# Kernel optimization log

Hardware: AMD Instinct MI355X
Metric: run time of the kernel (lower is better)

## Reference

```python
import jax, jax.numpy as jnp
import numpy as np

NUM_HEADS = 8
NUM_GROUPS = 8
EPS = 1e-5


def group_norm(x, scale, bias):
    # x: [B, C, H, W]; GroupNorm with NUM_GROUPS groups, per-channel affine.
    B, C, H, W = x.shape
    xg = x.reshape(B, NUM_GROUPS, C // NUM_GROUPS, H, W)
    mean = jnp.mean(xg, axis=(2, 3, 4), keepdims=True)
    var = jnp.var(xg, axis=(2, 3, 4), keepdims=True)
    xg = (xg - mean) * jax.lax.rsqrt(var + EPS)
    xn = xg.reshape(B, C, H, W)
    return xn * scale[None, :, None, None] + bias[None, :, None, None]


def setup_inputs() -> dict:
    key = jax.random.key(0)
    ks = jax.random.split(key, 4)
    B, C, H, W = 8, 256, 32, 32
    x = jax.random.normal(ks[0], (B, C, H, W), dtype=jnp.float32)
    gn_scale = jnp.ones((C,), dtype=jnp.float32)
    gn_bias = jnp.zeros((C,), dtype=jnp.float32)
    w_qkv = jax.random.normal(ks[1], (3 * C, C), dtype=jnp.float32) * (1.0 / np.sqrt(C))
    b_qkv = jnp.zeros((3 * C,), dtype=jnp.float32)
    w_out = jax.random.normal(ks[2], (C, C), dtype=jnp.float32) * (1.0 / np.sqrt(C))
    b_out = jnp.zeros((C,), dtype=jnp.float32)
    return {"x": x, "gn_scale": gn_scale, "gn_bias": gn_bias,
            "w_qkv": w_qkv, "b_qkv": b_qkv, "w_out": w_out, "b_out": b_out}


def reference(x, gn_scale, gn_bias, w_qkv, b_qkv, w_out, b_out):
    B, C, H, W = x.shape
    hd = C // NUM_HEADS  # head_dim
    N = H * W

    h = group_norm(x, gn_scale, gn_bias)
    # 1x1 conv == channel matmul: [B, 3C, H, W]
    qkv = jnp.einsum('oc,bchw->bohw', w_qkv, h) + b_qkv[None, :, None, None]
    q, k, v = jnp.split(qkv, 3, axis=1)
    # [B, heads, head_dim, N]
    q = q.reshape(B, NUM_HEADS, hd, N)
    k = k.reshape(B, NUM_HEADS, hd, N)
    v = v.reshape(B, NUM_HEADS, hd, N)

    scale = 1.0 / np.sqrt(hd).astype(np.float32)
    attn = jnp.einsum('bhdn,bhdm->bhnm', q, k) * scale  # [B, h, N, N]
    attn = jax.nn.softmax(attn, axis=-1)
    out = jnp.einsum('bhnm,bhdm->bhdn', attn, v)  # [B, h, hd, N]
    out = out.reshape(B, C, H, W)
    out = jnp.einsum('oc,bchw->bohw', w_out, out) + b_out[None, :, None, None]
    return x + out
```

## Files before the change

### kernel.cpp

```cpp
#include <hip/hip_runtime.h>
#include <hip/hip_bf16.h>
#include <math.h>

#define BB 8
#define CC 256
#define NN 1024
#define HEADS 8
#define HDIM 32
#define NGRP 8

using bf16x8 = __attribute__((ext_vector_type(8))) short;
using f32x4  = __attribute__((ext_vector_type(4))) float;

#if __has_builtin(__builtin_amdgcn_exp2f)
#define EXP2(x) __builtin_amdgcn_exp2f(x)
#else
#define EXP2(x) exp2f(x)
#endif

#define SCL_Q_LOG2E 0.2550348892803828f

static __device__ __forceinline__ ushort f2bf(float x) {
  union { __hip_bfloat16 b; ushort u; } c;
  c.b = __float2bfloat16(x);
  return c.u;
}

__global__ __launch_bounds__(256) void gn_stats1(
    const float* __restrict__ x, float2* __restrict__ part)
{
  const int p = blockIdx.x, t = threadIdx.x;
  const float4* src = (const float4*)x + (size_t)p * 512;
  const float4 a = src[t], b = src[t + 256];
  float s  = a.x + a.y + a.z + a.w + b.x + b.y + b.z + b.w;
  float ss = a.x*a.x + a.y*a.y + a.z*a.z + a.w*a.w
           + b.x*b.x + b.y*b.y + b.z*b.z + b.w*b.w;
#pragma unroll
  for (int off = 32; off > 0; off >>= 1) {
    s  += __shfl_down(s, off);
    ss += __shfl_down(ss, off);
  }
  __shared__ float rs[4], rss[4];
  const int wid = t >> 6, lane = t & 63;
  if (lane == 0) { rs[wid] = s; rss[wid] = ss; }
  __syncthreads();
  if (t == 0) {
    float2 o;
    o.x = rs[0] + rs[1] + rs[2] + rs[3];
    o.y = rss[0] + rss[1] + rss[2] + rss[3];
    part[p] = o;
  }
}

__global__ __launch_bounds__(256) void gnt_kernel(
    const float* __restrict__ x, const float2* __restrict__ part,
    const float* __restrict__ gns, const float* __restrict__ gnb,
    ushort* __restrict__ hT)
{
  __shared__ ushort Ls[64 * 68];
  __shared__ float2 gstat[2];
  const int t = threadIdx.x;
  const int b = blockIdx.z;
  const int c0 = blockIdx.y << 6, n0 = blockIdx.x << 6;

  if (t < 32) {
    const int gsel = t >> 4, ci = t & 15;
    const float2 pp = part[((b * 8) + (blockIdx.y << 1) + gsel) * 16 + ci];
    float s = pp.x, ss = pp.y;
#pragma unroll
    for (int off = 8; off > 0; off >>= 1) {
      s  += __shfl_down(s, off, 16);
      ss += __shfl_down(ss, off, 16);
    }
    if (ci == 0) {
      const float mean = s * (1.f / 32768.f);
      const float var = ss * (1.f / 32768.f) - mean * mean;
      float2 o; o.x = mean; o.y = rsqrtf(var + 1e-5f);
      gstat[gsel] = o;
    }
  }
  __syncthreads();

#pragma unroll
  for (int li = 0; li < 4; ++li) {
    const int id = t + (li << 8);
    const int row = id >> 4, col4 = id & 15;
    const int c = c0 + row;
    const float2 st = gstat[row >> 5];
    const float sc = gns[c] * st.y;
    const float sh = gnb[c] - st.x * sc;
    const float4 v = *(const float4*)(x + ((size_t)b * CC + c) * NN + n0 + col4 * 4);
    const int nb = col4 * 4;
    Ls[(nb + 0) * 68 + row] = f2bf(v.x * sc + sh);
    Ls[(nb + 1) * 68 + row] = f2bf(v.y * sc + sh);
    Ls[(nb + 2) * 68 + row] = f2bf(v.z * sc + sh);
    Ls[(nb + 3) * 68 + row] = f2bf(v.w * sc + sh);
  }
  __syncthreads();
#pragma unroll
  for (int li = 0; li < 2; ++li) {
    const int id = t + (li << 8);
    const int nR = id >> 3, cP = id & 7;
    union { uint4 v; ushort4 s[2]; } ov;
    ov.s[0] = *(const ushort4*)&Ls[nR * 68 + cP * 8];
    ov.s[1] = *(const ushort4*)&Ls[nR * 68 + cP * 8 + 4];
    *(uint4*)(hT + ((size_t)b * NN + n0 + nR) * CC + c0 + cP * 8) = ov.v;
  }
}

template <int MODE>
__global__ __launch_bounds__(256) void conv_mfma_kernel(
    const float* __restrict__ W32, const float* __restrict__ bias,
    const ushort* __restrict__ X, const float* __restrict__ xres,
    ushort* __restrict__ qT2, ushort* __restrict__ kT2, ushort* __restrict__ vN,
    float* __restrict__ out)
{
  const int t = threadIdx.x;
  const int w = t >> 6, l = t & 63;
  const int lg = l >> 4, lr = l & 15;
  const int wr = w >> 1, wc = w & 1;
  const int b = blockIdx.z;
  const int o0 = blockIdx.y << 6, n0 = blockIdx.x << 6;

  __shared__ ushort Ws[64][72];
  __shared__ ushort Xs[64][72];

  union FragU { ushort4 u[2]; bf16x8 f; };
  f32x4 acc[2][2] = {};

  const ushort* Xb = X + (size_t)b * 1024 * 256;

  for (int k0 = 0; k0 < 256; k0 += 64) {
    __syncthreads();
#pragma unroll
    for (int li = 0; li < 2; ++li) {
      const int id = t + (li << 8);
      const int rr = id >> 3, c8 = id & 7;
      const float* wsrc = W32 + (size_t)(o0 + rr) * 256 + k0 + c8 * 8;
      const float4 wa = *(const float4*)wsrc;
      const float4 wb = *(const float4*)(wsrc + 4);
      union { uint4 v; ushort s[8]; } wv;
      wv.s[0] = f2bf(wa.x); wv.s[1] = f2bf(wa.y); wv.s[2] = f2bf(wa.z); wv.s[3] = f2bf(wa.w);
      wv.s[4] = f2bf(wb.x); wv.s[5] = f2bf(wb.y); wv.s[6] = f2bf(wb.z); wv.s[7] = f2bf(wb.w);
      *(uint4*)&Ws[rr][c8 * 8] = wv.v;
      const uint4 xv = *(const uint4*)(Xb + (size_t)(n0 + rr) * 256 + k0 + c8 * 8);
      *(uint4*)&Xs[rr][c8 * 8] = xv;
    }
    __syncthreads();

    FragU af[2][2], xf[2][2];
#pragma unroll
    for (int i = 0; i < 2; ++i)
#pragma unroll
      for (int kc = 0; kc < 2; ++kc) {
        const ushort* p = &Ws[wr * 32 + i * 16 + lr][kc * 32 + lg * 4];
        af[i][kc].u[0] = *(const ushort4*)p;
        af[i][kc].u[1] = *(const ushort4*)(p + 16);
        const ushort* q = &Xs[wc * 32 + i * 16 + lr][kc * 32 + lg * 4];
        xf[i][kc].u[0] = *(const ushort4*)q;
        xf[i][kc].u[1] = *(const ushort4*)(q + 16);
      }
#pragma unroll
    for (int ms = 0; ms < 2; ++ms)
#pragma unroll
      for (int ns = 0; ns < 2; ++ns) {
        acc[ms][ns] = __builtin_amdgcn_mfma_f32_16x16x32_bf16(af[ms][0].f, xf[ns][0].f, acc[ms][ns], 0, 0, 0);
        acc[ms][ns] = __builtin_amdgcn_mfma_f32_16x16x32_bf16(af[ms][1].f, xf[ns][1].f, acc[ms][ns], 0, 0, 0);
      }
  }

  if (MODE == 0) {
    const int sec = o0 >> 8;
    const int oin = o0 & 255;
    const float scl = (sec == 0) ? SCL_Q_LOG2E : 1.0f;
    ushort* Lp = &Xs[0][0];
    __syncthreads();
#pragma unroll
    for (int ms = 0; ms < 2; ++ms) {
      const int ob = o0 + wr * 32 + ms * 16 + lg * 4;
      const float4 b4 = *(const float4*)(bias + ob);
      const int ol = wr * 32 + ms * 16 + lg * 4;
#pragma unroll
      for (int ns = 0; ns < 2; ++ns) {
        const int nl = wc * 32 + ns * 16 + lr;
        Lp[(ol + 0) * 68 + nl] = f2bf((acc[ms][ns][0] + b4.x) * scl);
        Lp[(ol + 1) * 68 + nl] = f2bf((acc[ms][ns][1] + b4.y) * scl);
        Lp[(ol + 2) * 68 + nl] = f2bf((acc[ms][ns][2] + b4.z) * scl);
        Lp[(ol + 3) * 68 + nl] = f2bf((acc[ms][ns][3] + b4.w) * scl);
      }
    }
    __syncthreads();
    if (sec < 2) {
      ushort* dst = (sec == 0) ? qT2 : kT2;
      const int nl = t & 63, hd = t >> 6;
      const int hl = hd >> 1, dh = hd & 1;
      const int bh = b * 8 + (oin >> 5) + hl;
      union { uint4 v[2]; ushort s[16]; } o;
#pragma unroll
      for (int j = 0; j < 16; ++j)
        o.s[j] = Lp[(hl * 32 + dh * 16 + j) * 68 + nl];
      uint4* dp = (uint4*)(dst + (((size_t)bh * 2 + dh) * 1024 + n0 + nl) * 16);
      dp[0] = o.v[0];
      dp[1] = o.v[1];
    } else {
      const int r = t >> 2, p = t & 3;
      const int oo = oin + r, hh = oo >> 5, d0 = oo & 31;
      union { uint4 v[2]; ushort4 s[4]; } o;
#pragma unroll
      for (int j = 0; j < 4; ++j)
        o.s[j] = *(const ushort4*)&Lp[r * 68 + p * 16 + j * 4];
      uint4* dp = (uint4*)(vN + (((size_t)b * 8 + hh) * 32 + d0) * 1024 + n0 + p * 16);
      dp[0] = o.v[0];
      dp[1] = o.v[1];
    }
  } else {
#pragma unroll
    for (int ms = 0; ms < 2; ++ms) {
      const int ob = o0 + wr * 32 + ms * 16 + lg * 4;
      const float4 b4 = *(const float4*)(bias + ob);
#pragma unroll
      for (int ns = 0; ns < 2; ++ns) {
        const int n = n0 + wc * 32 + ns * 16 + lr;
        const size_t i0 = ((size_t)b * 256 + ob) * 1024 + n;
        out[i0]          = acc[ms][ns][0] + b4.x + xres[i0];
        out[i0 + 1024]   = acc[ms][ns][1] + b4.y + xres[i0 + 1024];
        out[i0 + 2048]   = acc[ms][ns][2] + b4.z + xres[i0 + 2048];
        out[i0 + 3072]   = acc[ms][ns][3] + b4.w + xres[i0 + 3072];
      }
    }
  }
}

__global__ __launch_bounds__(128) void attn_kernel(
    const ushort* __restrict__ qT2, const ushort* __restrict__ kT2,
    const ushort* __restrict__ vN, ushort* __restrict__ aoT)
{
  const int t = threadIdx.x;
  const int w = t >> 6, l = t & 63;
  const int lg = l >> 4, lr = l & 15;
  const int bh = blockIdx.y;
  const int b = bh >> 3, hh = bh & 7;
  const int qbase = blockIdx.x << 6;

  __shared__ ushort Ks[64][40];
  __shared__ ushort Vs[32][72];

  union FragU { ushort4 u[2]; bf16x8 f; };

  const ushort* Qb2 = qT2 + (size_t)bh * 2 * 1024 * 16;
  const ushort* Kb2 = kT2 + (size_t)bh * 2 * 1024 * 16;
  const ushort* Vbh = vN + (size_t)bh * 32 * 1024;

  FragU qf[2];
#pragma unroll
  for (int qh = 0; qh < 2; ++qh) {
    const int qn = qbase + w * 32 + qh * 16 + lr;
    qf[qh].u[0] = *(const ushort4*)(Qb2 + (size_t)qn * 16 + lg * 4);
    qf[qh].u[1] = *(const ushort4*)(Qb2 + (size_t)(1024 + qn) * 16 + lg * 4);
  }

  f32x4 accO[2][2] = {};
  float lsum0 = 0.f, lsum1 = 0.f;

  const int km = t >> 1, kh = t & 1;
  const ushort* kbase = Kb2 + ((size_t)kh * 1024 + km) * 16;
  const int vd = t >> 2, vp = (t & 3) * 16;
  const ushort* vbase = Vbh + (size_t)vd * 1024 + vp;

  uint4 kr0 = *(const uint4*)kbase;
  uint4 kr1 = *(const uint4*)(kbase + 8);
  uint4 vr0 = *(const uint4*)vbase;
  uint4 vr1 = *(const uint4*)(vbase + 8);

  for (int m0 = 0; m0 < NN; m0 += 64) {
    __syncthreads();
    *(uint4*)&Ks[km][kh * 16] = kr0;
    *(uint4*)&Ks[km][kh * 16 + 8] = kr1;
    *(uint4*)&Vs[vd][vp] = vr0;
    *(uint4*)&Vs[vd][vp + 8] = vr1;
    __syncthreads();

    if (m0 + 64 < NN) {
      const ushort* kn = kbase + (size_t)(m0 + 64) * 16;
      kr0 = *(const uint4*)kn;
      kr1 = *(const uint4*)(kn + 8);
      const ushort* vn2 = vbase + (m0 + 64);
      vr0 = *(const uint4*)vn2;
      vr1 = *(const uint4*)(vn2 + 8);
    }

    f32x4 s[4][2];
#pragma unroll
    for (int ms = 0; ms < 4; ++ms) {
      FragU kf;
      const ushort* kp = &Ks[ms * 16 + lr][lg * 4];
      kf.u[0] = *(const ushort4*)kp;
      kf.u[1] = *(const ushort4*)(kp + 16);
      f32x4 z = {0.f, 0.f, 0.f, 0.f};
      s[ms][0] = __builtin_amdgcn_mfma_f32_16x16x32_bf16(kf.f, qf[0].f, z, 0, 0, 0);
      s[ms][1] = __builtin_amdgcn_mfma_f32_16x16x32_bf16(kf.f, qf[1].f, z, 0, 0, 0);
    }

    bf16x8 pb[2][2];
#pragma unroll
    for (int mc = 0; mc < 2; ++mc) {
      bf16x8 f0, f1;
#pragma unroll
      for (int r = 0; r < 4; ++r) {
        const float a0 = EXP2(s[2 * mc][0][r]);
        const float a1 = EXP2(s[2 * mc + 1][0][r]);
        const float b0 = EXP2(s[2 * mc][1][r]);
        const float b1 = EXP2(s[2 * mc + 1][1][r]);
        lsum0 += a0 + a1;
        lsum1 += b0 + b1;
        f0[r] = (short)f2bf(a0); f0[r + 4] = (short)f2bf(a1);
        f1[r] = (short)f2bf(b0); f1[r + 4] = (short)f2bf(b1);
      }
      pb[0][mc] = f0;
      pb[1][mc] = f1;
    }

#pragma unroll
    for (int dt = 0; dt < 2; ++dt) {
#pragma unroll
      for (int mc = 0; mc < 2; ++mc) {
        FragU vf;
        const ushort* vpp = &Vs[dt * 16 + lr][mc * 32 + lg * 4];
        vf.u[0] = *(const ushort4*)vpp;
        vf.u[1] = *(const ushort4*)(vpp + 16);
        accO[0][dt] = __builtin_amdgcn_mfma_f32_16x16x32_bf16(vf.f, pb[0][mc], accO[0][dt], 0, 0, 0);
        accO[1][dt] = __builtin_amdgcn_mfma_f32_16x16x32_bf16(vf.f, pb[1][mc], accO[1][dt], 0, 0, 0);
      }
    }
  }

  lsum0 += __shfl_xor(lsum0, 16); lsum0 += __shfl_xor(lsum0, 32);
  lsum1 += __shfl_xor(lsum1, 16); lsum1 += __shfl_xor(lsum1, 32);
  const float inv0 = 1.f / lsum0, inv1 = 1.f / lsum1;

  ushort* Lb = &Ks[0][0];
  __syncthreads();
#pragma unroll
  for (int dt = 0; dt < 2; ++dt)
#pragma unroll
    for (int r = 0; r < 4; ++r) {
      Lb[(w * 32 + lr) * 36 + dt * 16 + lg * 4 + r]      = f2bf(accO[0][dt][r] * inv0);
      Lb[(w * 32 + 16 + lr) * 36 + dt * 16 + lg * 4 + r] = f2bf(accO[1][dt][r] * inv1);
    }
  __syncthreads();
  {
    const int nl = t >> 1, pp = (t & 1) * 16;
    union { uint4 v[2]; ushort4 s[4]; } o;
#pragma unroll
    for (int j = 0; j < 4; ++j)
      o.s[j] = *(const ushort4*)&Lb[nl * 36 + pp + j * 4];
    uint4* dp = (uint4*)(aoT + ((size_t)b * 1024 + qbase + nl) * 256 + hh * 32 + pp);
    dp[0] = o.v[0];
    dp[1] = o.v[1];
  }
}

extern "C" void kernel_launch(void* const* d_in, const int* in_sizes, int n_in,
                              void* d_out, int out_size, void* d_ws, size_t ws_size,
                              hipStream_t stream)
{
  const float* x    = (const float*)d_in[0];
  const float* gns  = (const float*)d_in[1];
  const float* gnb  = (const float*)d_in[2];
  const float* wqkv = (const float*)d_in[3];
  const float* bqkv = (const float*)d_in[4];
  const float* wout = (const float*)d_in[5];
  const float* bout = (const float*)d_in[6];
  float* out = (float*)d_out;

  char* ws = (char*)d_ws;
  ushort* hT   = (ushort*)(ws);
  ushort* qT2  = (ushort*)(ws + (4u << 20));
  ushort* kT2  = (ushort*)(ws + (8u << 20));
  ushort* vN   = (ushort*)(ws + (12u << 20));
  ushort* aoT  = (ushort*)(ws + (16u << 20));
  float2* part = (float2*)(ws + (20u << 20));

  gn_stats1<<<dim3(1024), dim3(256), 0, stream>>>(x, part);
  gnt_kernel<<<dim3(16, 4, 8), dim3(256), 0, stream>>>(x, part, gns, gnb, hT);
  conv_mfma_kernel<0><<<dim3(16, 12, 8), dim3(256), 0, stream>>>(
      wqkv, bqkv, hT, nullptr, qT2, kT2, vN, nullptr);
  attn_kernel<<<dim3(16, 64), dim3(128), 0, stream>>>(qT2, kT2, vN, aoT);
  conv_mfma_kernel<1><<<dim3(16, 4, 8), dim3(256), 0, stream>>>(
      wout, bout, aoT, x, nullptr, nullptr, nullptr, out);
}
```

Measured before the change: 119.1 us.

## Fuse all five stages into one cooperative persistent kernel with grid syncs

Replaces the five separate launches (GN stats, GN+transpose, QKV conv, attention, output conv) with a single cooperative kernel of 512 blocks that runs each stage in turn, separated by grid.sync(). The aim is to remove per-launch overhead and inter-kernel gaps. The attention stage now uses 256-thread blocks covering 128 queries each, with adjusted K/V load mappings. In exchange it adds grid-wide barrier cost and fixes the grid at 512 blocks, which limits parallelism in the attention stage and requires all blocks to be co-resident.

```diff
diff --git a/kernel.cpp b/kernel.cpp
--- a/kernel.cpp
+++ b/kernel.cpp
@@ -1,6 +1,9 @@
 #include <hip/hip_runtime.h>
 #include <hip/hip_bf16.h>
+#include <hip/hip_cooperative_groups.h>
 #include <math.h>
+
+namespace cg = cooperative_groups;
 
 #define BB 8
 #define CC 256
@@ -26,108 +29,24 @@
   return c.u;
 }
 
-__global__ __launch_bounds__(256) void gn_stats1(
-    const float* __restrict__ x, float2* __restrict__ part)
-{
-  const int p = blockIdx.x, t = threadIdx.x;
-  const float4* src = (const float4*)x + (size_t)p * 512;
-  const float4 a = src[t], b = src[t + 256];
-  float s  = a.x + a.y + a.z + a.w + b.x + b.y + b.z + b.w;
-  float ss = a.x*a.x + a.y*a.y + a.z*a.z + a.w*a.w
-           + b.x*b.x + b.y*b.y + b.z*b.z + b.w*b.w;
-#pragma unroll
-  for (int off = 32; off > 0; off >>= 1) {
-    s  += __shfl_down(s, off);
-    ss += __shfl_down(ss, off);
-  }
-  __shared__ float rs[4], rss[4];
-  const int wid = t >> 6, lane = t & 63;
-  if (lane == 0) { rs[wid] = s; rss[wid] = ss; }
-  __syncthreads();
-  if (t == 0) {
-    float2 o;
-    o.x = rs[0] + rs[1] + rs[2] + rs[3];
-    o.y = rss[0] + rss[1] + rss[2] + rss[3];
-    part[p] = o;
-  }
-}
-
-__global__ __launch_bounds__(256) void gnt_kernel(
-    const float* __restrict__ x, const float2* __restrict__ part,
-    const float* __restrict__ gns, const float* __restrict__ gnb,
-    ushort* __restrict__ hT)
-{
-  __shared__ ushort Ls[64 * 68];
-  __shared__ float2 gstat[2];
-  const int t = threadIdx.x;
-  const int b = blockIdx.z;
-  const int c0 = blockIdx.y << 6, n0 = blockIdx.x << 6;
-
-  if (t < 32) {
-    const int gsel = t >> 4, ci = t & 15;
-    const float2 pp = part[((b * 8) + (blockIdx.y << 1) + gsel) * 16 + ci];
-    float s = pp.x, ss = pp.y;
-#pragma unroll
-    for (int off = 8; off > 0; off >>= 1) {
-      s  += __shfl_down(s, off, 16);
-      ss += __shfl_down(ss, off, 16);
-    }
-    if (ci == 0) {
-      const float mean = s * (1.f / 32768.f);
-      const float var = ss * (1.f / 32768.f) - mean * mean;
-      float2 o; o.x = mean; o.y = rsqrtf(var + 1e-5f);
-      gstat[gsel] = o;
-    }
-  }
-  __syncthreads();
-
-#pragma unroll
-  for (int li = 0; li < 4; ++li) {
-    const int id = t + (li << 8);
-    const int row = id >> 4, col4 = id & 15;
-    const int c = c0 + row;
-    const float2 st = gstat[row >> 5];
-    const float sc = gns[c] * st.y;
-    const float sh = gnb[c] - st.x * sc;
-    const float4 v = *(const float4*)(x + ((size_t)b * CC + c) * NN + n0 + col4 * 4);
-    const int nb = col4 * 4;
-    Ls[(nb + 0) * 68 + row] = f2bf(v.x * sc + sh);
-    Ls[(nb + 1) * 68 + row] = f2bf(v.y * sc + sh);
-    Ls[(nb + 2) * 68 + row] = f2bf(v.z * sc + sh);
-    Ls[(nb + 3) * 68 + row] = f2bf(v.w * sc + sh);
-  }
-  __syncthreads();
-#pragma unroll
-  for (int li = 0; li < 2; ++li) {
-    const int id = t + (li << 8);
-    const int nR = id >> 3, cP = id & 7;
-    union { uint4 v; ushort4 s[2]; } ov;
-    ov.s[0] = *(const ushort4*)&Ls[nR * 68 + cP * 8];
-    ov.s[1] = *(const ushort4*)&Ls[nR * 68 + cP * 8 + 4];
-    *(uint4*)(hT + ((size_t)b * NN + n0 + nR) * CC + c0 + cP * 8) = ov.v;
-  }
-}
+union FragU { ushort4 u[2]; bf16x8 f; };
 
 template <int MODE>
-__global__ __launch_bounds__(256) void conv_mfma_kernel(
+static __device__ __forceinline__ void conv_tile(
+    char* smem, const int t, const int b, const int o0, const int n0,
     const float* __restrict__ W32, const float* __restrict__ bias,
     const ushort* __restrict__ X, const float* __restrict__ xres,
-    ushort* __restrict__ qT2, ushort* __restrict__ kT2, ushort* __restrict__ vN,
-    float* __restrict__ out)
+    ushort* __restrict__ qT2, ushort* __restrict__ kT2,
+    ushort* __restrict__ vN, float* __restrict__ out)
 {
-  const int t = threadIdx.x;
   const int w = t >> 6, l = t & 63;
   const int lg = l >> 4, lr = l & 15;
   const int wr = w >> 1, wc = w & 1;
-  const int b = blockIdx.z;
-  const int o0 = blockIdx.y << 6, n0 = blockIdx.x << 6;
-
-  __shared__ ushort Ws[64][72];
-  __shared__ ushort Xs[64][72];
-
-  union FragU { ushort4 u[2]; bf16x8 f; };
+
+  ushort (*Ws)[72] = (ushort(*)[72])smem;
+  ushort (*Xs)[72] = (ushort(*)[72])(smem + 9216);
+
   f32x4 acc[2][2] = {};
-
   const ushort* Xb = X + (size_t)b * 1024 * 256;
 
   for (int k0 = 0; k0 < 256; k0 += 64) {
@@ -231,132 +150,229 @@
   }
 }
 
-__global__ __launch_bounds__(128) void attn_kernel(
-    const ushort* __restrict__ qT2, const ushort* __restrict__ kT2,
-    const ushort* __restrict__ vN, ushort* __restrict__ aoT)
+__global__ __launch_bounds__(256, 2) void fused_kernel(
+    const float* __restrict__ x, const float* __restrict__ gns,
+    const float* __restrict__ gnb, const float* __restrict__ wqkv,
+    const float* __restrict__ bqkv, const float* __restrict__ wout,
+    const float* __restrict__ bout, float* __restrict__ out,
+    ushort* __restrict__ hT, ushort* __restrict__ qT2,
+    ushort* __restrict__ kT2, ushort* __restrict__ vN,
+    ushort* __restrict__ aoT, float2* __restrict__ part)
 {
+  cg::grid_group grid = cg::this_grid();
+  __shared__ __align__(16) char smem[18432];
+  __shared__ float rs[4], rss[4];
+  __shared__ float2 gstat[2];
   const int t = threadIdx.x;
-  const int w = t >> 6, l = t & 63;
-  const int lg = l >> 4, lr = l & 15;
-  const int bh = blockIdx.y;
-  const int b = bh >> 3, hh = bh & 7;
-  const int qbase = blockIdx.x << 6;
-
-  __shared__ ushort Ks[64][40];
-  __shared__ ushort Vs[32][72];
-
-  union FragU { ushort4 u[2]; bf16x8 f; };
-
-  const ushort* Qb2 = qT2 + (size_t)bh * 2 * 1024 * 16;
-  const ushort* Kb2 = kT2 + (size_t)bh * 2 * 1024 * 16;
-  const ushort* Vbh = vN + (size_t)bh * 32 * 1024;
-
-  FragU qf[2];
-#pragma unroll
-  for (int qh = 0; qh < 2; ++qh) {
-    const int qn = qbase + w * 32 + qh * 16 + lr;
-    qf[qh].u[0] = *(const ushort4*)(Qb2 + (size_t)qn * 16 + lg * 4);
-    qf[qh].u[1] = *(const ushort4*)(Qb2 + (size_t)(1024 + qn) * 16 + lg * 4);
-  }
-
-  f32x4 accO[2][2] = {};
-  float lsum0 = 0.f, lsum1 = 0.f;
-
-  const int km = t >> 1, kh = t & 1;
-  const ushort* kbase = Kb2 + ((size_t)kh * 1024 + km) * 16;
-  const int vd = t >> 2, vp = (t & 3) * 16;
-  const ushort* vbase = Vbh + (size_t)vd * 1024 + vp;
-
-  uint4 kr0 = *(const uint4*)kbase;
-  uint4 kr1 = *(const uint4*)(kbase + 8);
-  uint4 vr0 = *(const uint4*)vbase;
-  uint4 vr1 = *(const uint4*)(vbase + 8);
-
-  for (int m0 = 0; m0 < NN; m0 += 64) {
-    __syncthreads();
-    *(uint4*)&Ks[km][kh * 16] = kr0;
-    *(uint4*)&Ks[km][kh * 16 + 8] = kr1;
-    *(uint4*)&Vs[vd][vp] = vr0;
-    *(uint4*)&Vs[vd][vp + 8] = vr1;
-    __syncthreads();
-
-    if (m0 + 64 < NN) {
-      const ushort* kn = kbase + (size_t)(m0 + 64) * 16;
-      kr0 = *(const uint4*)kn;
-      kr1 = *(const uint4*)(kn + 8);
-      const ushort* vn2 = vbase + (m0 + 64);
-      vr0 = *(const uint4*)vn2;
-      vr1 = *(const uint4*)(vn2 + 8);
-    }
-
-    f32x4 s[4][2];
-#pragma unroll
-    for (int ms = 0; ms < 4; ++ms) {
-      FragU kf;
-      const ushort* kp = &Ks[ms * 16 + lr][lg * 4];
-      kf.u[0] = *(const ushort4*)kp;
-      kf.u[1] = *(const ushort4*)(kp + 16);
-      f32x4 z = {0.f, 0.f, 0.f, 0.f};
-      s[ms][0] = __builtin_amdgcn_mfma_f32_16x16x32_bf16(kf.f, qf[0].f, z, 0, 0, 0);
-      s[ms][1] = __builtin_amdgcn_mfma_f32_16x16x32_bf16(kf.f, qf[1].f, z, 0, 0, 0);
-    }
-
-    bf16x8 pb[2][2];
-#pragma unroll
-    for (int mc = 0; mc < 2; ++mc) {
-      bf16x8 f0, f1;
+  const int bid = blockIdx.x;
+  const int wid = t >> 6, lane = t & 63;
+
+#pragma unroll
+  for (int ci = 0; ci < 2; ++ci) {
+    const int c = bid + ci * 512;
+    const float4* src = (const float4*)x + (size_t)c * 512;
+    const float4 a = src[t], b2 = src[t + 256];
+    float s  = a.x + a.y + a.z + a.w + b2.x + b2.y + b2.z + b2.w;
+    float ss = a.x*a.x + a.y*a.y + a.z*a.z + a.w*a.w
+             + b2.x*b2.x + b2.y*b2.y + b2.z*b2.z + b2.w*b2.w;
+#pragma unroll
+    for (int off = 32; off > 0; off >>= 1) {
+      s  += __shfl_down(s, off);
+      ss += __shfl_down(ss, off);
+    }
+    __syncthreads();
+    if (lane == 0) { rs[wid] = s; rss[wid] = ss; }
+    __syncthreads();
+    if (t == 0) {
+      float2 o;
+      o.x = rs[0] + rs[1] + rs[2] + rs[3];
+      o.y = rss[0] + rss[1] + rss[2] + rss[3];
+      part[c] = o;
+    }
+  }
+  grid.sync();
+
+  {
+    const int b = bid >> 6;
+    const int cq = (bid >> 4) & 3;
+    const int c0 = cq << 6, n0 = (bid & 15) << 6;
+    ushort* Ls = (ushort*)smem;
+
+    if (t < 32) {
+      const int gsel = t >> 4, ci = t & 15;
+      const float2 pp = part[((b * 8) + (cq << 1) + gsel) * 16 + ci];
+      float s = pp.x, ss = pp.y;
+#pragma unroll
+      for (int off = 8; off > 0; off >>= 1) {
+        s  += __shfl_down(s, off, 16);
+        ss += __shfl_down(ss, off, 16);
+      }
+      if (ci == 0) {
+        const float mean = s * (1.f / 32768.f);
+        const float var = ss * (1.f / 32768.f) - mean * mean;
+        float2 o; o.x = mean; o.y = rsqrtf(var + 1e-5f);
+        gstat[gsel] = o;
+      }
+    }
+    __syncthreads();
+
+#pragma unroll
+    for (int li = 0; li < 4; ++li) {
+      const int id = t + (li << 8);
+      const int row = id >> 4, col4 = id & 15;
+      const int c = c0 + row;
+      const float2 st = gstat[row >> 5];
+      const float sc = gns[c] * st.y;
+      const float sh = gnb[c] - st.x * sc;
+      const float4 v = *(const float4*)(x + ((size_t)b * CC + c) * NN + n0 + col4 * 4);
+      const int nb = col4 * 4;
+      Ls[(nb + 0) * 68 + row] = f2bf(v.x * sc + sh);
+      Ls[(nb + 1) * 68 + row] = f2bf(v.y * sc + sh);
+      Ls[(nb + 2) * 68 + row] = f2bf(v.z * sc + sh);
+      Ls[(nb + 3) * 68 + row] = f2bf(v.w * sc + sh);
+    }
+    __syncthreads();
+#pragma unroll
+    for (int li = 0; li < 2; ++li) {
+      const int id = t + (li << 8);
+      const int nR = id >> 3, cP = id & 7;
+      union { uint4 v; ushort4 s[2]; } ov;
+      ov.s[0] = *(const ushort4*)&Ls[nR * 68 + cP * 8];
+      ov.s[1] = *(const ushort4*)&Ls[nR * 68 + cP * 8 + 4];
+      *(uint4*)(hT + ((size_t)b * NN + n0 + nR) * CC + c0 + cP * 8) = ov.v;
+    }
+  }
+  grid.sync();
+
+  for (int u = bid; u < 1536; u += 512) {
+    const int nx = u & 15;
+    const int v = u >> 4;
+    const int b = v / 12;
+    const int oy = v - b * 12;
+    conv_tile<0>(smem, t, b, oy << 6, nx << 6, wqkv, bqkv, hT, nullptr,
+                 qT2, kT2, vN, nullptr);
+  }
+  grid.sync();
+
+  {
+    const int w = t >> 6, l = t & 63;
+    const int lg = l >> 4, lr = l & 15;
+    const int bh = bid >> 3;
+    const int b = bh >> 3, hh = bh & 7;
+    const int qb = (bid & 7) << 7;
+
+    ushort* Ks = (ushort*)smem;
+    ushort* Vs = (ushort*)(smem + 10240);
+
+    const ushort* Qb2 = qT2 + (size_t)bh * 2 * 1024 * 16;
+    const ushort* Kb2 = kT2 + (size_t)bh * 2 * 1024 * 16;
+    const ushort* Vbh = vN + (size_t)bh * 32 * 1024;
+
+    FragU qf[2];
+#pragma unroll
+    for (int qh = 0; qh < 2; ++qh) {
+      const int qn = qb + w * 32 + qh * 16 + lr;
+      qf[qh].u[0] = *(const ushort4*)(Qb2 + (size_t)qn * 16 + lg * 4);
+      qf[qh].u[1] = *(const ushort4*)(Qb2 + (size_t)(1024 + qn) * 16 + lg * 4);
+    }
+
+    f32x4 accO[2][2] = {};
+    float lsum0 = 0.f, lsum1 = 0.f;
+
+    const int km = t >> 2, ksel = t & 3, kdh = ksel >> 1, khalf = ksel & 1;
+    const ushort* kbase = Kb2 + ((size_t)kdh * 1024 + km) * 16 + khalf * 8;
+    const int vd = t >> 3, vm = (t & 7) * 8;
+    const ushort* vbase = Vbh + (size_t)vd * 1024 + vm;
+
+    uint4 kr = *(const uint4*)kbase;
+    uint4 vr = *(const uint4*)vbase;
+
+    for (int m0 = 0; m0 < NN; m0 += 64) {
+      __syncthreads();
+      *(uint4*)&Ks[km * 40 + kdh * 16 + khalf * 8] = kr;
+      *(uint4*)&Vs[vd * 72 + vm] = vr;
+      __syncthreads();
+      if (m0 + 64 < NN) {
+        kr = *(const uint4*)(kbase + (size_t)(m0 + 64) * 16);
+        vr = *(const uint4*)(vbase + (m0 + 64));
+      }
+
+      f32x4 s[4][2];
+#pragma unroll
+      for (int ms = 0; ms < 4; ++ms) {
+        FragU kf;
+        const ushort* kp = &Ks[(ms * 16 + lr) * 40 + lg * 4];
+        kf.u[0] = *(const ushort4*)kp;
+        kf.u[1] = *(const ushort4*)(kp + 16);
+        f32x4 z = {0.f, 0.f, 0.f, 0.f};
+        s[ms][0] = __builtin_amdgcn_mfma_f32_16x16x32_bf16(kf.f, qf[0].f, z, 0, 0, 0);
+        s[ms][1] = __builtin_amdgcn_mfma_f32_16x16x32_bf16(kf.f, qf[1].f, z, 0, 0, 0);
+      }
+
+      bf16x8 pb[2][2];
+#pragma unroll
+      for (int mc = 0; mc < 2; ++mc) {
+        bf16x8 f0, f1;
+#pragma unroll
+        for (int r = 0; r < 4; ++r) {
+          const float a0 = EXP2(s[2 * mc][0][r]);
+          const float a1 = EXP2(s[2 * mc + 1][0][r]);
+          const float b0 = EXP2(s[2 * mc][1][r]);
+          const float b1 = EXP2(s[2 * mc + 1][1][r]);
+          lsum0 += a0 + a1;
+          lsum1 += b0 + b1;
+          f0[r] = (short)f2bf(a0); f0[r + 4] = (short)f2bf(a1);
+          f1[r] = (short)f2bf(b0); f1[r + 4] = (short)f2bf(b1);
+        }
+        pb[0][mc] = f0;
+        pb[1][mc] = f1;
+      }
+
+#pragma unroll
+      for (int dt = 0; dt < 2; ++dt) {
+#pragma unroll
+        for (int mc = 0; mc < 2; ++mc) {
+          FragU vf;
+          const ushort* vpp = &Vs[(dt * 16 + lr) * 72 + mc * 32 + lg * 4];
+          vf.u[0] = *(const ushort4*)vpp;
+          vf.u[1] = *(const ushort4*)(vpp + 16);
+          accO[0][dt] = __builtin_amdgcn_mfma_f32_16x16x32_bf16(vf.f, pb[0][mc], accO[0][dt], 0, 0, 0);
+          accO[1][dt] = __builtin_amdgcn_mfma_f32_16x16x32_bf16(vf.f, pb[1][mc], accO[1][dt], 0, 0, 0);
+        }
+      }
+    }
+
+    lsum0 += __shfl_xor(lsum0, 16); lsum0 += __shfl_xor(lsum0, 32);
+    lsum1 += __shfl_xor(lsum1, 16); lsum1 += __shfl_xor(lsum1, 32);
+    const float inv0 = 1.f / lsum0, inv1 = 1.f / lsum1;
+
+    ushort* Lb = (ushort*)smem;
+    __syncthreads();
+#pragma unroll
+    for (int dt = 0; dt < 2; ++dt)
 #pragma unroll
       for (int r = 0; r < 4; ++r) {
-        const float a0 = EXP2(s[2 * mc][0][r]);
-        const float a1 = EXP2(s[2 * mc + 1][0][r]);
-        const float b0 = EXP2(s[2 * mc][1][r]);
-        const float b1 = EXP2(s[2 * mc + 1][1][r]);
-        lsum0 += a0 + a1;
-        lsum1 += b0 + b1;
-        f0[r] = (short)f2bf(a0); f0[r + 4] = (short)f2bf(a1);
-        f1[r] = (short)f2bf(b0); f1[r + 4] = (short)f2bf(b1);
-      }
-      pb[0][mc] = f0;
-      pb[1][mc] = f1;
-    }
-
-#pragma unroll
-    for (int dt = 0; dt < 2; ++dt) {
-#pragma unroll
-      for (int mc = 0; mc < 2; ++mc) {
-        FragU vf;
-        const ushort* vpp = &Vs[dt * 16 + lr][mc * 32 + lg * 4];
-        vf.u[0] = *(const ushort4*)vpp;
-        vf.u[1] = *(const ushort4*)(vpp + 16);
-        accO[0][dt] = __builtin_amdgcn_mfma_f32_16x16x32_bf16(vf.f, pb[0][mc], accO[0][dt], 0, 0, 0);
-        accO[1][dt] = __builtin_amdgcn_mfma_f32_16x16x32_bf16(vf.f, pb[1][mc], accO[1][dt], 0, 0, 0);
-      }
-    }
-  }
-
-  lsum0 += __shfl_xor(lsum0, 16); lsum0 += __shfl_xor(lsum0, 32);
-  lsum1 += __shfl_xor(lsum1, 16); lsum1 += __shfl_xor(lsum1, 32);
-  const float inv0 = 1.f / lsum0, inv1 = 1.f / lsum1;
-
-  ushort* Lb = &Ks[0][0];
-  __syncthreads();
-#pragma unroll
-  for (int dt = 0; dt < 2; ++dt)
-#pragma unroll
-    for (int r = 0; r < 4; ++r) {
-      Lb[(w * 32 + lr) * 36 + dt * 16 + lg * 4 + r]      = f2bf(accO[0][dt][r] * inv0);
-      Lb[(w * 32 + 16 + lr) * 36 + dt * 16 + lg * 4 + r] = f2bf(accO[1][dt][r] * inv1);
-    }
-  __syncthreads();
+        Lb[(w * 32 + lr) * 36 + dt * 16 + lg * 4 + r]      = f2bf(accO[0][dt][r] * inv0);
+        Lb[(w * 32 + 16 + lr) * 36 + dt * 16 + lg * 4 + r] = f2bf(accO[1][dt][r] * inv1);
+      }
+    __syncthreads();
+    {
+      const int nl = t >> 1, pp = (t & 1) * 16;
+      union { uint4 v[2]; ushort4 s[4]; } o;
+#pragma unroll
+      for (int j = 0; j < 4; ++j)
+        o.s[j] = *(const ushort4*)&Lb[nl * 36 + pp + j * 4];
+      uint4* dp = (uint4*)(aoT + ((size_t)b * 1024 + qb + nl) * 256 + hh * 32 + pp);
+      dp[0] = o.v[0];
+      dp[1] = o.v[1];
+    }
+  }
+  grid.sync();
+
   {
-    const int nl = t >> 1, pp = (t & 1) * 16;
-    union { uint4 v[2]; ushort4 s[4]; } o;
-#pragma unroll
-    for (int j = 0; j < 4; ++j)
-      o.s[j] = *(const ushort4*)&Lb[nl * 36 + pp + j * 4];
-    uint4* dp = (uint4*)(aoT + ((size_t)b * 1024 + qbase + nl) * 256 + hh * 32 + pp);
-    dp[0] = o.v[0];
-    dp[1] = o.v[1];
+    const int nx = bid & 15, oy = (bid >> 4) & 3, b = bid >> 6;
+    conv_tile<1>(smem, t, b, oy << 6, nx << 6, wout, bout, aoT, x,
+                 nullptr, nullptr, nullptr, out);
   }
 }
 
@@ -381,11 +397,11 @@
   ushort* aoT  = (ushort*)(ws + (16u << 20));
   float2* part = (float2*)(ws + (20u << 20));
 
-  gn_stats1<<<dim3(1024), dim3(256), 0, stream>>>(x, part);
-  gnt_kernel<<<dim3(16, 4, 8), dim3(256), 0, stream>>>(x, part, gns, gnb, hT);
-  conv_mfma_kernel<0><<<dim3(16, 12, 8), dim3(256), 0, stream>>>(
-      wqkv, bqkv, hT, nullptr, qT2, kT2, vN, nullptr);
-  attn_kernel<<<dim3(16, 64), dim3(128), 0, stream>>>(qT2, kT2, vN, aoT);
-  conv_mfma_kernel<1><<<dim3(16, 4, 8), dim3(256), 0, stream>>>(
-      wout, bout, aoT, x, nullptr, nullptr, nullptr, out);
+  void* args[] = {
+    (void*)&x, (void*)&gns, (void*)&gnb, (void*)&wqkv, (void*)&bqkv,
+    (void*)&wout, (void*)&bout, (void*)&out, (void*)&hT, (void*)&qT2,
+    (void*)&kT2, (void*)&vN, (void*)&aoT, (void*)&part
+  };
+  hipLaunchCooperativeKernel((const void*)fused_kernel, dim3(512), dim3(256),
+                             args, 0, stream);
 }
```

After: 343.3 us. 2.88x slower.
